# Performance work log

Hardware: AMD Instinct MI355X
Metric: run time of the kernel (lower is better)

Reference implementation:

```python
import jax, jax.numpy as jnp
import numpy as np

B, CIN, COUT, H, W = 2, 64, 64, 192, 192
G = 2          # offset groups (region + semantic offset branches concatenated)
KK = 9         # 3x3 kernel taps
CG = CIN // G  # channels per offset group


def conv2d(x, w, b):
    # NCHW, OIHW, stride 1, padding 1 (same as nn.Conv2d(k=3, s=1, p=1))
    y = jax.lax.conv_general_dilated(x, w, (1, 1), ((1, 1), (1, 1)),
                                     dimension_numbers=('NCHW', 'OIHW', 'NCHW'))
    return y + b[None, :, None, None]


def bilinear_gather(x, py, px):
    # x: (B,G,C,H,W); py,px: (B,G,K,H,W) absolute sample coords (float)
    b, g, c, h, w = x.shape
    k = py.shape[2]
    y0 = jnp.floor(py)
    x0 = jnp.floor(px)
    ly = (py - y0)[:, :, None]   # (B,G,1,K,H,W)
    lx = (px - x0)[:, :, None]
    xf = x.reshape(b, g, c, h * w)

    def corner(yi, xi):
        valid = (yi >= 0) & (yi < h) & (xi >= 0) & (xi < w)
        idx = (jnp.clip(yi, 0, h - 1).astype(jnp.int32) * w
               + jnp.clip(xi, 0, w - 1).astype(jnp.int32))          # (B,G,K,H,W)
        idxf = idx.reshape(b, g, k * h * w)
        gat = jax.vmap(jax.vmap(lambda xc, ic: jnp.take(xc, ic, axis=1)))(xf, idxf)
        gat = gat.reshape(b, g, c, k, h, w)
        return gat * valid[:, :, None].astype(x.dtype)

    v00 = corner(y0, x0)
    v01 = corner(y0, x0 + 1)
    v10 = corner(y0 + 1, x0)
    v11 = corner(y0 + 1, x0 + 1)
    return (v00 * (1 - ly) * (1 - lx) + v01 * (1 - ly) * lx
            + v10 * ly * (1 - lx) + v11 * ly * lx)


def setup_inputs() -> dict:
    key = jax.random.key(0)
    ks = jax.random.split(key, 12)
    stdv = 1.0 / np.sqrt(CIN * 9)
    inp = {
        'input': jax.random.normal(ks[0], (B, CIN, H, W), jnp.float32),
        'mask_in': jax.random.uniform(ks[1], (B, 1, H, W), jnp.float32),
        'weight': jax.random.uniform(ks[2], (COUT, CIN, 3, 3), jnp.float32, -stdv, stdv),
        'bias': jnp.zeros((COUT,), jnp.float32),
        'sem_w': jax.random.normal(ks[3], (2 * KK, CIN, 3, 3), jnp.float32) * 0.01,
        'sem_b': jnp.zeros((2 * KK,), jnp.float32),
        'reg_w': jax.random.normal(ks[4], (2 * KK, 1, 3, 3), jnp.float32) * 0.01,
        'reg_b': jnp.zeros((2 * KK,), jnp.float32),
        'm1_w': jax.random.normal(ks[5], (KK, 1, 3, 3), jnp.float32) * 0.1,
        'm1_b': jnp.zeros((KK,), jnp.float32),
        'm2_w': jax.random.normal(ks[6], (KK, CIN, 3, 3), jnp.float32) * 0.1,
        'm2_b': jnp.zeros((KK,), jnp.float32),
    }
    return inp


def reference(input, mask_in, weight, bias, sem_w, sem_b, reg_w, reg_b,
              m1_w, m1_b, m2_w, m2_b):
    f32 = input.dtype
    # --- learned offsets: region (group 0) then semantic (group 1) ---
    region_offset = conv2d(mask_in, reg_w, reg_b)    # (B, 2*9, H, W)
    semantic_offset = conv2d(input, sem_w, sem_b)    # (B, 2*9, H, W)
    offset = jnp.concatenate([region_offset, semantic_offset], axis=1)
    off = offset.reshape(B, G, KK, 2, H, W)          # [..., 0]=dy, [..., 1]=dx
    ky = (jnp.arange(KK) // 3 - 1).astype(f32)[None, None, :, None, None]
    kx = (jnp.arange(KK) % 3 - 1).astype(f32)[None, None, :, None, None]
    gy = jnp.arange(H, dtype=f32)[None, None, None, :, None]
    gx = jnp.arange(W, dtype=f32)[None, None, None, None, :]
    py = off[:, :, :, 0] + gy + ky                   # (B,G,K,H,W)
    px = off[:, :, :, 1] + gx + kx

    # --- update mask: deform conv of repeated mask with all-ones weight (no grad) ---
    # mask repeated over CIN channels -> identical within each offset group, so
    # sample one channel per group and scale: out = 2 (out chans) * CG * sum_{g,k}
    mgrp = jnp.broadcast_to(mask_in[:, None], (B, G, 1, H, W))
    sm = bilinear_gather(mgrp, py, px)               # (B,G,1,K,H,W)
    update_mask = jnp.clip(2.0 * CG * sm.sum(axis=(1, 2, 3)), 0.0, 1.0)[:, None]
    update_mask = jax.lax.stop_gradient(update_mask)  # (B,1,H,W)

    # --- modulation masks ---
    dm1 = jax.nn.sigmoid(conv2d(mask_in, m1_w, m1_b))  # (B,9,H,W) -> group 0
    dm2 = jax.nn.sigmoid(conv2d(input, m2_w, m2_b))    # (B,9,H,W) -> group 1
    dmask = jnp.concatenate([dm1, dm2], axis=1).reshape(B, G, KK, H, W)[:, :, None]

    # --- main modulated deformable conv ---
    xg = input.reshape(B, G, CG, H, W)
    sampled = bilinear_gather(xg, py, px) * dmask    # (B,G,CG,K,H,W)
    wr = weight.reshape(COUT, G, CG, KK)
    raw = jnp.einsum('bgckhw,ogck->bohw', sampled, wr) + bias[None, :, None, None]

    output = raw * update_mask
    return output, update_mask
```

## Files before the change

kernel.cpp:

```cpp
#include <hip/hip_runtime.h>
#include <hip/hip_bf16.h>
#include <math.h>

#define B_  2
#define CIN 64
#define COUT 64
#define H_  192
#define W_  192
#define G_  2
#define KK_ 9
#define CG_ 32
#define HW_ (H_*W_)
#define PIX 32
#define XT_ (W_/PIX)
#define PR_ 7
#define PC_ 38
#define PST 72
#define NB_NHWC (B_ * (HW_ / 64))
#define NB_WT   ((18*4*64*8 + 18*2*64*8) / 256)

typedef __attribute__((ext_vector_type(8))) short bf16x8;
typedef __attribute__((ext_vector_type(4))) float f32x4;

static __device__ __forceinline__ short f2bf(float f) {
    unsigned u = __builtin_bit_cast(unsigned, f);
    u = (u + 0x7fffu + ((u >> 16) & 1u)) >> 16;
    return (short)u;
}
static __device__ __forceinline__ float bf2f(short s) {
    unsigned u = ((unsigned)(unsigned short)s) << 16;
    return __builtin_bit_cast(float, u);
}
static __device__ __forceinline__ short2 pk2bf(float lo, float hi) {
    float2 f; f.x = lo; f.y = hi;
    __hip_bfloat162 hh = __float22bfloat162_rn(f);
    short2 r;
    __builtin_memcpy(&r, &hh, sizeof(r));
    return r;
}

__global__ __launch_bounds__(256)
void prep_kernel(const float* __restrict__ in,
                 const float* __restrict__ weight,
                 const float* __restrict__ sem_w,
                 const float* __restrict__ m2_w,
                 short* __restrict__ inpT,
                 short* __restrict__ wbm,
                 short* __restrict__ wbs) {
    __shared__ float t[64][65];
    const int tid = threadIdx.x;
    const int bid = blockIdx.x;
    if (bid < NB_NHWC) {
        const int b = bid / (HW_ / 64);
        const int pix0 = (bid % (HW_ / 64)) * 64;
        const float* src = in + (size_t)b * CIN * HW_ + pix0;
        const int c0 = (tid >> 6) * 16;
        const int p  = tid & 63;
        #pragma unroll
        for (int i = 0; i < 16; ++i)
            t[c0 + i][p] = src[(size_t)(c0 + i) * HW_ + p];
        __syncthreads();
        short* dst = inpT + ((size_t)b * HW_ + pix0) * 64;
        #pragma unroll
        for (int i = 0; i < 2; ++i) {
            int item = i * 256 + tid;
            int pp = item >> 3, oct = item & 7;
            bf16x8 v;
            #pragma unroll
            for (int j = 0; j < 8; j += 2) {
                short2 ss = pk2bf(t[oct * 8 + j][pp], t[oct * 8 + j + 1][pp]);
                v[j] = ss.x; v[j + 1] = ss.y;
            }
            *(bf16x8*)&dst[pp * 64 + oct * 8] = v;
        }
        return;
    }
    int i = (bid - NB_NHWC) * 256 + tid;
    if (i < 18 * 4 * 64 * 8) {
        int j = i & 7, lane = (i >> 3) & 63, nt = (i >> 9) & 3, gk = i >> 11;
        int n = lane & 15, q = lane >> 4;
        int o = nt * 16 + n;
        int g = gk / 9, k = gk - g * 9;
        int cin = g * CG_ + q * 8 + j;
        wbm[i] = f2bf(weight[(o * CIN + cin) * 9 + k]);
        return;
    }
    int ii = i - 18 * 4 * 64 * 8;
    if (ii >= 18 * 2 * 64 * 8) return;
    int j = ii & 7, lane = (ii >> 3) & 63, nt = (ii >> 9) & 1, s = ii >> 10;
    int t_ = s >> 1, h = s & 1;
    int n = lane & 15, q = lane >> 4;
    int o = nt * 16 + n;
    int c = h * 32 + q * 8 + j;
    float v = 0.f;
    if (o < 18)      v = sem_w[(o * CIN + c) * 9 + t_];
    else if (o < 27) v = m2_w[((o - 18) * CIN + c) * 9 + t_];
    wbs[ii] = f2bf(v);
}

#define MSTEP(GK) { \
    uint4 mt0 = meta[(GK) * 32 + n]; \
    uint4 mt1 = meta[(GK) * 32 + 16 + n]; \
    const short* pb = patch + team * 32 + q * 8; \
    bf16x8 d00 = *(const bf16x8*)&pb[(mt0.z & 0xffffu) * PST]; \
    bf16x8 d01 = *(const bf16x8*)&pb[(mt0.z >> 16) * PST]; \
    bf16x8 d10 = *(const bf16x8*)&pb[(mt0.w & 0xffffu) * PST]; \
    bf16x8 d11 = *(const bf16x8*)&pb[(mt0.w >> 16) * PST]; \
    bf16x8 e00 = *(const bf16x8*)&pb[(mt1.z & 0xffffu) * PST]; \
    bf16x8 e01 = *(const bf16x8*)&pb[(mt1.z >> 16) * PST]; \
    bf16x8 e10 = *(const bf16x8*)&pb[(mt1.w & 0xffffu) * PST]; \
    bf16x8 e11 = *(const bf16x8*)&pb[(mt1.w >> 16) * PST]; \
    float v00 = bf2f((short)(mt0.x & 0xffffu)); \
    float v01 = bf2f((short)(mt0.x >> 16)); \
    float v10 = bf2f((short)(mt0.y & 0xffffu)); \
    float v11 = bf2f((short)(mt0.y >> 16)); \
    float u00 = bf2f((short)(mt1.x & 0xffffu)); \
    float u01 = bf2f((short)(mt1.x >> 16)); \
    float u10 = bf2f((short)(mt1.y & 0xffffu)); \
    float u11 = bf2f((short)(mt1.y >> 16)); \
    bf16x8 a0, a1; \
    _Pragma("unroll") \
    for (int j = 0; j < 8; j += 2) { \
        float s0 = v00 * bf2f(d00[j])   + v01 * bf2f(d01[j]) \
                 + v10 * bf2f(d10[j])   + v11 * bf2f(d11[j]); \
        float s1 = v00 * bf2f(d00[j+1]) + v01 * bf2f(d01[j+1]) \
                 + v10 * bf2f(d10[j+1]) + v11 * bf2f(d11[j+1]); \
        short2 ss = pk2bf(s0, s1); \
        a0[j] = ss.x; a0[j + 1] = ss.y; \
        float t0 = u00 * bf2f(e00[j])   + u01 * bf2f(e01[j]) \
                 + u10 * bf2f(e10[j])   + u11 * bf2f(e11[j]); \
        float t1 = u00 * bf2f(e00[j+1]) + u01 * bf2f(e01[j+1]) \
                 + u10 * bf2f(e10[j+1]) + u11 * bf2f(e11[j+1]); \
        short2 tt = pk2bf(t0, t1); \
        a1[j] = tt.x; a1[j + 1] = tt.y; \
    } \
    bf16x8 wb0 = ((const bf16x8*)wbm)[((GK) * 4 + 0) * 64 + lane]; \
    bf16x8 wb1 = ((const bf16x8*)wbm)[((GK) * 4 + 1) * 64 + lane]; \
    bf16x8 wb2 = ((const bf16x8*)wbm)[((GK) * 4 + 2) * 64 + lane]; \
    bf16x8 wb3 = ((const bf16x8*)wbm)[((GK) * 4 + 3) * 64 + lane]; \
    ma00 = __builtin_amdgcn_mfma_f32_16x16x32_bf16(a0, wb0, ma00, 0, 0, 0); \
    ma01 = __builtin_amdgcn_mfma_f32_16x16x32_bf16(a0, wb1, ma01, 0, 0, 0); \
    ma02 = __builtin_amdgcn_mfma_f32_16x16x32_bf16(a0, wb2, ma02, 0, 0, 0); \
    ma03 = __builtin_amdgcn_mfma_f32_16x16x32_bf16(a0, wb3, ma03, 0, 0, 0); \
    ma10 = __builtin_amdgcn_mfma_f32_16x16x32_bf16(a1, wb0, ma10, 0, 0, 0); \
    ma11 = __builtin_amdgcn_mfma_f32_16x16x32_bf16(a1, wb1, ma11, 0, 0, 0); \
    ma12 = __builtin_amdgcn_mfma_f32_16x16x32_bf16(a1, wb2, ma12, 0, 0, 0); \
    ma13 = __builtin_amdgcn_mfma_f32_16x16x32_bf16(a1, wb3, ma13, 0, 0, 0); \
}

#define DUMP(OP) { \
    _Pragma("unroll") \
    for (int r = 0; r < 4; ++r) { \
        dout[(q * 4 + r) * 68 +  0 + n] OP ma00[r]; \
        dout[(q * 4 + r) * 68 + 16 + n] OP ma01[r]; \
        dout[(q * 4 + r) * 68 + 32 + n] OP ma02[r]; \
        dout[(q * 4 + r) * 68 + 48 + n] OP ma03[r]; \
        dout[(16 + q * 4 + r) * 68 +  0 + n] OP ma10[r]; \
        dout[(16 + q * 4 + r) * 68 + 16 + n] OP ma11[r]; \
        dout[(16 + q * 4 + r) * 68 + 32 + n] OP ma12[r]; \
        dout[(16 + q * 4 + r) * 68 + 48 + n] OP ma13[r]; \
    } \
}

__global__ __launch_bounds__(256)
void fused_kernel(const short* __restrict__ inpT,
                  const float* __restrict__ mask_in,
                  const short* __restrict__ wbs,
                  const short* __restrict__ wbm,
                  const float* __restrict__ sem_b,
                  const float* __restrict__ reg_w, const float* __restrict__ reg_b,
                  const float* __restrict__ m1_w, const float* __restrict__ m1_b,
                  const float* __restrict__ m2_b,
                  const float* __restrict__ bias,
                  float* __restrict__ out, float* __restrict__ um_out) {
    __shared__ __align__(16) short patch[PR_ * PC_ * PST];
    __shared__ __align__(16) char sh[9216];
    __shared__ uint4 meta[18 * 32];
    __shared__ float ums[4 * 32];
    __shared__ float umv[32];
    float* red  = (float*)sh;
    float* dout = (float*)sh;

    const int tid  = threadIdx.x;
    const int lane = tid & 63;
    const int w    = __builtin_amdgcn_readfirstlane(tid >> 6);
    const int team = w >> 1;
    const int kh   = w & 1;
    const int n = lane & 15, q = lane >> 4;

    const int bid  = blockIdx.x;
    const int band = bid & 7;
    const int jb   = bid >> 3;
    const int xt   = jb % XT_;
    const int rr   = band * 48 + jb / XT_;
    const int y    = rr % H_;
    const int b    = rr / H_;
    const int x0   = xt * PIX;

    for (int i = tid; i < PR_ * PC_ * 8; i += 256) {
        int chunk = i & 7;
        int cc = (i >> 3) % PC_;
        int rp = (i >> 3) / PC_;
        int yy = y - 3 + rp;
        int xx = x0 - 3 + cc;
        bf16x8 v = {0, 0, 0, 0, 0, 0, 0, 0};
        if (yy >= 0 && yy < H_ && xx >= 0 && xx < W_)
            v = *(const bf16x8*)&inpT[((size_t)(b * HW_ + yy * W_ + xx)) * 64 + chunk * 8];
        *(bf16x8*)&patch[(rp * PC_ + cc) * PST + chunk * 8] = v;
    }
    __syncthreads();

    f32x4 acc0 = {0.f, 0.f, 0.f, 0.f}, acc1 = {0.f, 0.f, 0.f, 0.f};
    for (int ss = 0; ss < 9; ++ss) {
        int s = team * 9 + ss;
        int tt = s >> 1, hh = s & 1;
        int dy = tt / 3 - 1, dx = tt % 3 - 1;
        int r = dy + 3;
        int c = kh * 16 + n + dx + 3;
        bf16x8 a = *(const bf16x8*)&patch[(r * PC_ + c) * PST + hh * 32 + q * 8];
        bf16x8 b0 = ((const bf16x8*)wbs)[(s * 2 + 0) * 64 + lane];
        bf16x8 b1 = ((const bf16x8*)wbs)[(s * 2 + 1) * 64 + lane];
        acc0 = __builtin_amdgcn_mfma_f32_16x16x32_bf16(a, b0, acc0, 0, 0, 0);
        acc1 = __builtin_amdgcn_mfma_f32_16x16x32_bf16(a, b1, acc1, 0, 0, 0);
    }
    #pragma unroll
    for (int r = 0; r < 4; ++r) {
        red[team * 1152 + (kh * 16 + q * 4 + r) * 36 + n]      = acc0[r];
        red[team * 1152 + (kh * 16 + q * 4 + r) * 36 + 16 + n] = acc1[r];
    }
    __syncthreads();

    if (w < 2) {
        const int g    = w;
        const int half = lane >> 5;
        const int pxl  = lane & 31;
        const int xl   = x0 + pxl;
        const int pixl = y * W_ + xl;
        const bool vxm = xl > 0, vxp = (xl + 1) < W_;
        const bool vym = y > 0,  vyp = (y + 1) < H_;
        const int k0 = half ? 5 : 0;
        const int k1 = half ? 9 : 5;
        float off_[18], mm[9];
        if (g == 0) {
            const float* mbp = mask_in + (size_t)b * HW_ + pixl;
            float mv[9];
            mv[0] = (vym && vxm) ? mbp[-W_ - 1] : 0.f;
            mv[1] = vym ? mbp[-W_] : 0.f;
            mv[2] = (vym && vxp) ? mbp[-W_ + 1] : 0.f;
            mv[3] = vxm ? mbp[-1] : 0.f;
            mv[4] = mbp[0];
            mv[5] = vxp ? mbp[1] : 0.f;
            mv[6] = (vyp && vxm) ? mbp[W_ - 1] : 0.f;
            mv[7] = vyp ? mbp[W_] : 0.f;
            mv[8] = (vyp && vxp) ? mbp[W_ + 1] : 0.f;
            #pragma unroll
            for (int o = 0; o < 18; ++o) off_[o] = reg_b[o];
            #pragma unroll
            for (int o = 0; o < 9; ++o) mm[o] = m1_b[o];
            #pragma unroll
            for (int t = 0; t < 9; ++t) {
                float vt = mv[t];
                #pragma unroll
                for (int o = 0; o < 18; ++o) off_[o] += vt * reg_w[o * 9 + t];
                #pragma unroll
                for (int o = 0; o < 9; ++o) mm[o] += vt * m1_w[o * 9 + t];
            }
        } else {
            #pragma unroll
            for (int o = 0; o < 18; ++o)
                off_[o] = red[pxl * 36 + o] + red[1152 + pxl * 36 + o] + sem_b[o];
            #pragma unroll
            for (int o = 0; o < 9; ++o)
                mm[o] = red[pxl * 36 + 18 + o] + red[1152 + pxl * 36 + 18 + o] + m2_b[o];
        }

        const float* mb = mask_in + (size_t)b * HW_;
        float s_um = 0.f;
        #pragma unroll
        for (int k = 0; k < 9; ++k) {
            if (k < k0 || k >= k1) continue;
            float Y = off_[2 * k]     + (float)y  + (float)(k / 3 - 1);
            float X = off_[2 * k + 1] + (float)xl + (float)(k % 3 - 1);
            int gk = g * 9 + k;
            float dm = 1.f / (1.f + expf(-mm[k]));
            float y0f = floorf(Y), x0f = floorf(X);
            int yi0 = (int)y0f, xi0 = (int)x0f;
            float ly = Y - y0f, lx = X - x0f;
            int yi1 = yi0 + 1, xi1 = xi0 + 1;
            bool vy0 = (yi0 >= 0 && yi0 < H_), vy1 = (yi1 >= 0 && yi1 < H_);
            bool vx0 = (xi0 >= 0 && xi0 < W_), vx1 = (xi1 >= 0 && xi1 < W_);
            float w00f = (vy0 && vx0) ? (1.f - ly) * (1.f - lx) : 0.f;
            float w01f = (vy0 && vx1) ? (1.f - ly) * lx : 0.f;
            float w10f = (vy1 && vx0) ? ly * (1.f - lx) : 0.f;
            float w11f = (vy1 && vx1) ? ly * lx : 0.f;
            int yc0 = min(max(yi0, 0), H_ - 1), yc1 = min(max(yi1, 0), H_ - 1);
            int xc0 = min(max(xi0, 0), W_ - 1), xc1 = min(max(xi1, 0), W_ - 1);
            s_um += w00f * mb[yc0 * W_ + xc0] + w01f * mb[yc0 * W_ + xc1]
                  + w10f * mb[yc1 * W_ + xc0] + w11f * mb[yc1 * W_ + xc1];
            int r0 = min(max(yc0 - (y - 3), 0), PR_ - 1);
            int r1 = min(max(yc1 - (y - 3), 0), PR_ - 1);
            int c0 = min(max(xc0 - (x0 - 3), 0), PC_ - 1);
            int c1 = min(max(xc1 - (x0 - 3), 0), PC_ - 1);
            short2 p01 = pk2bf(w00f * dm, w01f * dm);
            short2 p23 = pk2bf(w10f * dm, w11f * dm);
            uint4 mt;
            mt.x = (unsigned)(unsigned short)p01.x | ((unsigned)(unsigned short)p01.y << 16);
            mt.y = (unsigned)(unsigned short)p23.x | ((unsigned)(unsigned short)p23.y << 16);
            mt.z = (unsigned)(r0 * PC_ + c0) | ((unsigned)(r0 * PC_ + c1) << 16);
            mt.w = (unsigned)(r1 * PC_ + c0) | ((unsigned)(r1 * PC_ + c1) << 16);
            meta[gk * 32 + pxl] = mt;
        }
        ums[(g * 2 + half) * 32 + pxl] = s_um;
    }
    __syncthreads();
    if (tid < 32) {
        float s = ums[tid] + ums[32 + tid] + ums[64 + tid] + ums[96 + tid];
        float u = fminf(fmaxf(64.f * s, 0.f), 1.f);
        um_out[(size_t)b * HW_ + y * W_ + x0 + tid] = u;
        umv[tid] = u;
    }
    __syncthreads();

    f32x4 ma00 = {0.f,0.f,0.f,0.f}, ma01 = {0.f,0.f,0.f,0.f};
    f32x4 ma02 = {0.f,0.f,0.f,0.f}, ma03 = {0.f,0.f,0.f,0.f};
    f32x4 ma10 = {0.f,0.f,0.f,0.f}, ma11 = {0.f,0.f,0.f,0.f};
    f32x4 ma12 = {0.f,0.f,0.f,0.f}, ma13 = {0.f,0.f,0.f,0.f};
    {
        const int t9 = team * 9;
        if (kh == 0) {
            MSTEP(t9 + 0) MSTEP(t9 + 1) MSTEP(t9 + 2) MSTEP(t9 + 3) MSTEP(t9 + 4)
        } else {
            MSTEP(t9 + 5) MSTEP(t9 + 6) MSTEP(t9 + 7) MSTEP(t9 + 8)
        }
    }

    if (w == 3) DUMP(=)
    __syncthreads();
    if (w == 2) DUMP(+=)
    __syncthreads();
    if (w == 1) DUMP(+=)
    __syncthreads();
    if (w == 0) DUMP(+=)
    __syncthreads();

    {
        const int pxs = tid & 31;
        const int o0  = (tid >> 5) * 8;
        float u = umv[pxs];
        float* ob = out + ((size_t)b * COUT + o0) * HW_ + y * W_ + x0 + pxs;
        const float* bs = bias + o0;
        const float* dp = &dout[pxs * 68 + o0];
        #pragma unroll
        for (int o = 0; o < 8; ++o)
            ob[(size_t)o * HW_] = (dp[o] + bs[o]) * u;
    }
}

extern "C" void kernel_launch(void* const* d_in, const int* in_sizes, int n_in,
                              void* d_out, int out_size, void* d_ws, size_t ws_size,
                              hipStream_t stream) {
    const float* input   = (const float*)d_in[0];
    const float* mask_in = (const float*)d_in[1];
    const float* weight  = (const float*)d_in[2];
    const float* bias    = (const float*)d_in[3];
    const float* sem_w   = (const float*)d_in[4];
    const float* sem_b   = (const float*)d_in[5];
    const float* reg_w   = (const float*)d_in[6];
    const float* reg_b   = (const float*)d_in[7];
    const float* m1_w    = (const float*)d_in[8];
    const float* m1_b    = (const float*)d_in[9];
    const float* m2_w    = (const float*)d_in[10];
    const float* m2_b    = (const float*)d_in[11];

    float* out = (float*)d_out;
    float* um  = out + (size_t)B_ * COUT * HW_;

    short* inpT = (short*)d_ws;
    short* wbm  = inpT + (size_t)B_ * HW_ * 64;
    short* wbs  = wbm + 18 * 4 * 64 * 8;

    prep_kernel<<<NB_NHWC + NB_WT, 256, 0, stream>>>(
        input, weight, sem_w, m2_w, inpT, wbm, wbs);
    fused_kernel<<<B_ * H_ * XT_, 256, 0, stream>>>(
        inpT, mask_in, wbs, wbm, sem_b, reg_w, reg_b, m1_w, m1_b, m2_b,
        bias, out, um);
}
```

Before: 151.5 us.

## Switch to fp16 with packed half2 bilinear math and restructure meta/reduction

Converts input and weight staging from bf16 to fp16 so the bilinear interpolation runs as packed half2 FMAs and the MFMAs use the f16 variant. Shrinks per-sample metadata to packed half weights plus a single 16-bit patch index, deriving the other three corners from fixed offsets. Spreads offset/meta computation across all four waves instead of two, and replaces the serialized four-step accumulation dump with per-wave slices reused in the patch buffer and summed in the epilogue. It also switches to fast exp and reduces mask sums with a shuffle. Risks include fp16 range and precision loss, and clamping the corner index to PR-2/PC-2 may differ at borders.

New measurement: 139.5 us. -7.9%, faster.

```diff
diff --git a/kernel.cpp b/kernel.cpp
--- a/kernel.cpp
+++ b/kernel.cpp
@@ -1,5 +1,5 @@
 #include <hip/hip_runtime.h>
-#include <hip/hip_bf16.h>
+#include <hip/hip_fp16.h>
 #include <math.h>
 
 #define B_  2
@@ -16,27 +16,35 @@
 #define PR_ 7
 #define PC_ 38
 #define PST 72
+#define DSTR 69
 #define NB_NHWC (B_ * (HW_ / 64))
 #define NB_WT   ((18*4*64*8 + 18*2*64*8) / 256)
 
 typedef __attribute__((ext_vector_type(8))) short bf16x8;
+typedef __attribute__((ext_vector_type(8))) _Float16 f16x8;
+typedef __attribute__((ext_vector_type(4))) unsigned int u32x4;
 typedef __attribute__((ext_vector_type(4))) float f32x4;
 
-static __device__ __forceinline__ short f2bf(float f) {
-    unsigned u = __builtin_bit_cast(unsigned, f);
-    u = (u + 0x7fffu + ((u >> 16) & 1u)) >> 16;
-    return (short)u;
-}
-static __device__ __forceinline__ float bf2f(short s) {
-    unsigned u = ((unsigned)(unsigned short)s) << 16;
-    return __builtin_bit_cast(float, u);
-}
-static __device__ __forceinline__ short2 pk2bf(float lo, float hi) {
-    float2 f; f.x = lo; f.y = hi;
-    __hip_bfloat162 hh = __float22bfloat162_rn(f);
-    short2 r;
-    __builtin_memcpy(&r, &hh, sizeof(r));
-    return r;
+static __device__ __forceinline__ short f2h(float f) {
+    _Float16 h = (_Float16)f;
+    return __builtin_bit_cast(short, h);
+}
+static __device__ __forceinline__ unsigned pk2hu(float lo, float hi) {
+    auto h = __builtin_amdgcn_cvt_pkrtz(lo, hi);
+    return __builtin_bit_cast(unsigned, h);
+}
+static __device__ __forceinline__ short2 pk2h(float lo, float hi) {
+    auto h = __builtin_amdgcn_cvt_pkrtz(lo, hi);
+    return __builtin_bit_cast(short2, h);
+}
+static __device__ __forceinline__ __half2 bcl(unsigned u) {
+    return __builtin_bit_cast(__half2, (unsigned)((u & 0xffffu) | (u << 16)));
+}
+static __device__ __forceinline__ __half2 bch(unsigned u) {
+    return __builtin_bit_cast(__half2, (unsigned)((u >> 16) | (u & 0xffff0000u)));
+}
+static __device__ __forceinline__ __half2 H2(unsigned u) {
+    return __builtin_bit_cast(__half2, u);
 }
 
 __global__ __launch_bounds__(256)
@@ -68,7 +76,7 @@
             bf16x8 v;
             #pragma unroll
             for (int j = 0; j < 8; j += 2) {
-                short2 ss = pk2bf(t[oct * 8 + j][pp], t[oct * 8 + j + 1][pp]);
+                short2 ss = pk2h(t[oct * 8 + j][pp], t[oct * 8 + j + 1][pp]);
                 v[j] = ss.x; v[j + 1] = ss.y;
             }
             *(bf16x8*)&dst[pp * 64 + oct * 8] = v;
@@ -82,7 +90,7 @@
         int o = nt * 16 + n;
         int g = gk / 9, k = gk - g * 9;
         int cin = g * CG_ + q * 8 + j;
-        wbm[i] = f2bf(weight[(o * CIN + cin) * 9 + k]);
+        wbm[i] = f2h(weight[(o * CIN + cin) * 9 + k]);
         return;
     }
     int ii = i - 18 * 4 * 64 * 8;
@@ -95,70 +103,63 @@
     float v = 0.f;
     if (o < 18)      v = sem_w[(o * CIN + c) * 9 + t_];
     else if (o < 27) v = m2_w[((o - 18) * CIN + c) * 9 + t_];
-    wbs[ii] = f2bf(v);
+    wbs[ii] = f2h(v);
 }
 
 #define MSTEP(GK) { \
-    uint4 mt0 = meta[(GK) * 32 + n]; \
-    uint4 mt1 = meta[(GK) * 32 + 16 + n]; \
+    const uint2 mw0 = meta_w[(GK) * 32 + n]; \
+    const uint2 mw1 = meta_w[(GK) * 32 + 16 + n]; \
+    const int i0 = (int)meta_i[(GK) * 32 + n] * PST; \
+    const int i1 = (int)meta_i[(GK) * 32 + 16 + n] * PST; \
     const short* pb = patch + team * 32 + q * 8; \
-    bf16x8 d00 = *(const bf16x8*)&pb[(mt0.z & 0xffffu) * PST]; \
-    bf16x8 d01 = *(const bf16x8*)&pb[(mt0.z >> 16) * PST]; \
-    bf16x8 d10 = *(const bf16x8*)&pb[(mt0.w & 0xffffu) * PST]; \
-    bf16x8 d11 = *(const bf16x8*)&pb[(mt0.w >> 16) * PST]; \
-    bf16x8 e00 = *(const bf16x8*)&pb[(mt1.z & 0xffffu) * PST]; \
-    bf16x8 e01 = *(const bf16x8*)&pb[(mt1.z >> 16) * PST]; \
-    bf16x8 e10 = *(const bf16x8*)&pb[(mt1.w & 0xffffu) * PST]; \
-    bf16x8 e11 = *(const bf16x8*)&pb[(mt1.w >> 16) * PST]; \
-    float v00 = bf2f((short)(mt0.x & 0xffffu)); \
-    float v01 = bf2f((short)(mt0.x >> 16)); \
-    float v10 = bf2f((short)(mt0.y & 0xffffu)); \
-    float v11 = bf2f((short)(mt0.y >> 16)); \
-    float u00 = bf2f((short)(mt1.x & 0xffffu)); \
-    float u01 = bf2f((short)(mt1.x >> 16)); \
-    float u10 = bf2f((short)(mt1.y & 0xffffu)); \
-    float u11 = bf2f((short)(mt1.y >> 16)); \
-    bf16x8 a0, a1; \
+    u32x4 d00 = *(const u32x4*)&pb[i0]; \
+    u32x4 d01 = *(const u32x4*)&pb[i0 + PST]; \
+    u32x4 d10 = *(const u32x4*)&pb[i0 + PC_ * PST]; \
+    u32x4 d11 = *(const u32x4*)&pb[i0 + (PC_ + 1) * PST]; \
+    u32x4 e00 = *(const u32x4*)&pb[i1]; \
+    u32x4 e01 = *(const u32x4*)&pb[i1 + PST]; \
+    u32x4 e10 = *(const u32x4*)&pb[i1 + PC_ * PST]; \
+    u32x4 e11 = *(const u32x4*)&pb[i1 + (PC_ + 1) * PST]; \
+    __half2 v00 = bcl(mw0.x), v01 = bch(mw0.x), v10 = bcl(mw0.y), v11 = bch(mw0.y); \
+    __half2 u00 = bcl(mw1.x), u01 = bch(mw1.x), u10 = bcl(mw1.y), u11 = bch(mw1.y); \
+    u32x4 ra, rb; \
     _Pragma("unroll") \
-    for (int j = 0; j < 8; j += 2) { \
-        float s0 = v00 * bf2f(d00[j])   + v01 * bf2f(d01[j]) \
-                 + v10 * bf2f(d10[j])   + v11 * bf2f(d11[j]); \
-        float s1 = v00 * bf2f(d00[j+1]) + v01 * bf2f(d01[j+1]) \
-                 + v10 * bf2f(d10[j+1]) + v11 * bf2f(d11[j+1]); \
-        short2 ss = pk2bf(s0, s1); \
-        a0[j] = ss.x; a0[j + 1] = ss.y; \
-        float t0 = u00 * bf2f(e00[j])   + u01 * bf2f(e01[j]) \
-                 + u10 * bf2f(e10[j])   + u11 * bf2f(e11[j]); \
-        float t1 = u00 * bf2f(e00[j+1]) + u01 * bf2f(e01[j+1]) \
-                 + u10 * bf2f(e10[j+1]) + u11 * bf2f(e11[j+1]); \
-        short2 tt = pk2bf(t0, t1); \
-        a1[j] = tt.x; a1[j + 1] = tt.y; \
+    for (int jj = 0; jj < 4; ++jj) { \
+        __half2 s = __hfma2(H2(d00[jj]), v00, __hfma2(H2(d01[jj]), v01, \
+                    __hfma2(H2(d10[jj]), v10, __hmul2(H2(d11[jj]), v11)))); \
+        ra[jj] = __builtin_bit_cast(unsigned, s); \
+        __half2 t = __hfma2(H2(e00[jj]), u00, __hfma2(H2(e01[jj]), u01, \
+                    __hfma2(H2(e10[jj]), u10, __hmul2(H2(e11[jj]), u11)))); \
+        rb[jj] = __builtin_bit_cast(unsigned, t); \
     } \
-    bf16x8 wb0 = ((const bf16x8*)wbm)[((GK) * 4 + 0) * 64 + lane]; \
-    bf16x8 wb1 = ((const bf16x8*)wbm)[((GK) * 4 + 1) * 64 + lane]; \
-    bf16x8 wb2 = ((const bf16x8*)wbm)[((GK) * 4 + 2) * 64 + lane]; \
-    bf16x8 wb3 = ((const bf16x8*)wbm)[((GK) * 4 + 3) * 64 + lane]; \
-    ma00 = __builtin_amdgcn_mfma_f32_16x16x32_bf16(a0, wb0, ma00, 0, 0, 0); \
-    ma01 = __builtin_amdgcn_mfma_f32_16x16x32_bf16(a0, wb1, ma01, 0, 0, 0); \
-    ma02 = __builtin_amdgcn_mfma_f32_16x16x32_bf16(a0, wb2, ma02, 0, 0, 0); \
-    ma03 = __builtin_amdgcn_mfma_f32_16x16x32_bf16(a0, wb3, ma03, 0, 0, 0); \
-    ma10 = __builtin_amdgcn_mfma_f32_16x16x32_bf16(a1, wb0, ma10, 0, 0, 0); \
-    ma11 = __builtin_amdgcn_mfma_f32_16x16x32_bf16(a1, wb1, ma11, 0, 0, 0); \
-    ma12 = __builtin_amdgcn_mfma_f32_16x16x32_bf16(a1, wb2, ma12, 0, 0, 0); \
-    ma13 = __builtin_amdgcn_mfma_f32_16x16x32_bf16(a1, wb3, ma13, 0, 0, 0); \
-}
-
-#define DUMP(OP) { \
+    f16x8 a0 = __builtin_bit_cast(f16x8, ra); \
+    f16x8 a1 = __builtin_bit_cast(f16x8, rb); \
+    f16x8 wb0 = ((const f16x8*)wbm)[((GK) * 4 + 0) * 64 + lane]; \
+    f16x8 wb1 = ((const f16x8*)wbm)[((GK) * 4 + 1) * 64 + lane]; \
+    f16x8 wb2 = ((const f16x8*)wbm)[((GK) * 4 + 2) * 64 + lane]; \
+    f16x8 wb3 = ((const f16x8*)wbm)[((GK) * 4 + 3) * 64 + lane]; \
+    ma00 = __builtin_amdgcn_mfma_f32_16x16x32_f16(a0, wb0, ma00, 0, 0, 0); \
+    ma01 = __builtin_amdgcn_mfma_f32_16x16x32_f16(a0, wb1, ma01, 0, 0, 0); \
+    ma02 = __builtin_amdgcn_mfma_f32_16x16x32_f16(a0, wb2, ma02, 0, 0, 0); \
+    ma03 = __builtin_amdgcn_mfma_f32_16x16x32_f16(a0, wb3, ma03, 0, 0, 0); \
+    ma10 = __builtin_amdgcn_mfma_f32_16x16x32_f16(a1, wb0, ma10, 0, 0, 0); \
+    ma11 = __builtin_amdgcn_mfma_f32_16x16x32_f16(a1, wb1, ma11, 0, 0, 0); \
+    ma12 = __builtin_amdgcn_mfma_f32_16x16x32_f16(a1, wb2, ma12, 0, 0, 0); \
+    ma13 = __builtin_amdgcn_mfma_f32_16x16x32_f16(a1, wb3, ma13, 0, 0, 0); \
+}
+
+#define DUMP() { \
+    float* dw = dout + w * (32 * DSTR); \
     _Pragma("unroll") \
     for (int r = 0; r < 4; ++r) { \
-        dout[(q * 4 + r) * 68 +  0 + n] OP ma00[r]; \
-        dout[(q * 4 + r) * 68 + 16 + n] OP ma01[r]; \
-        dout[(q * 4 + r) * 68 + 32 + n] OP ma02[r]; \
-        dout[(q * 4 + r) * 68 + 48 + n] OP ma03[r]; \
-        dout[(16 + q * 4 + r) * 68 +  0 + n] OP ma10[r]; \
-        dout[(16 + q * 4 + r) * 68 + 16 + n] OP ma11[r]; \
-        dout[(16 + q * 4 + r) * 68 + 32 + n] OP ma12[r]; \
-        dout[(16 + q * 4 + r) * 68 + 48 + n] OP ma13[r]; \
+        dw[(q * 4 + r) * DSTR +  0 + n] = ma00[r]; \
+        dw[(q * 4 + r) * DSTR + 16 + n] = ma01[r]; \
+        dw[(q * 4 + r) * DSTR + 32 + n] = ma02[r]; \
+        dw[(q * 4 + r) * DSTR + 48 + n] = ma03[r]; \
+        dw[(16 + q * 4 + r) * DSTR +  0 + n] = ma10[r]; \
+        dw[(16 + q * 4 + r) * DSTR + 16 + n] = ma11[r]; \
+        dw[(16 + q * 4 + r) * DSTR + 32 + n] = ma12[r]; \
+        dw[(16 + q * 4 + r) * DSTR + 48 + n] = ma13[r]; \
     } \
 }
 
@@ -174,12 +175,12 @@
                   const float* __restrict__ bias,
                   float* __restrict__ out, float* __restrict__ um_out) {
     __shared__ __align__(16) short patch[PR_ * PC_ * PST];
-    __shared__ __align__(16) char sh[9216];
-    __shared__ uint4 meta[18 * 32];
+    __shared__ __align__(16) float red[2 * 32 * 36];
+    __shared__ __align__(8) uint2 meta_w[18 * 32];
+    __shared__ unsigned short meta_i[18 * 32];
     __shared__ float ums[4 * 32];
     __shared__ float umv[32];
-    float* red  = (float*)sh;
-    float* dout = (float*)sh;
+    float* dout = (float*)patch;
 
     const int tid  = threadIdx.x;
     const int lane = tid & 63;
@@ -217,11 +218,11 @@
         int dy = tt / 3 - 1, dx = tt % 3 - 1;
         int r = dy + 3;
         int c = kh * 16 + n + dx + 3;
-        bf16x8 a = *(const bf16x8*)&patch[(r * PC_ + c) * PST + hh * 32 + q * 8];
-        bf16x8 b0 = ((const bf16x8*)wbs)[(s * 2 + 0) * 64 + lane];
-        bf16x8 b1 = ((const bf16x8*)wbs)[(s * 2 + 1) * 64 + lane];
-        acc0 = __builtin_amdgcn_mfma_f32_16x16x32_bf16(a, b0, acc0, 0, 0, 0);
-        acc1 = __builtin_amdgcn_mfma_f32_16x16x32_bf16(a, b1, acc1, 0, 0, 0);
+        f16x8 a = *(const f16x8*)&patch[(r * PC_ + c) * PST + hh * 32 + q * 8];
+        f16x8 b0 = ((const f16x8*)wbs)[(s * 2 + 0) * 64 + lane];
+        f16x8 b1 = ((const f16x8*)wbs)[(s * 2 + 1) * 64 + lane];
+        acc0 = __builtin_amdgcn_mfma_f32_16x16x32_f16(a, b0, acc0, 0, 0, 0);
+        acc1 = __builtin_amdgcn_mfma_f32_16x16x32_f16(a, b1, acc1, 0, 0, 0);
     }
     #pragma unroll
     for (int r = 0; r < 4; ++r) {
@@ -230,16 +231,17 @@
     }
     __syncthreads();
 
-    if (w < 2) {
-        const int g    = w;
+    {
+        const int g    = team;
         const int half = lane >> 5;
         const int pxl  = lane & 31;
         const int xl   = x0 + pxl;
         const int pixl = y * W_ + xl;
         const bool vxm = xl > 0, vxp = (xl + 1) < W_;
         const bool vym = y > 0,  vyp = (y + 1) < H_;
-        const int k0 = half ? 5 : 0;
-        const int k1 = half ? 9 : 5;
+        const int qk = (kh << 1) | half;
+        const int k0 = (qk == 0) ? 0 : (qk == 1) ? 3 : (qk == 2) ? 5 : 7;
+        const int k1 = (qk == 0) ? 3 : (qk == 1) ? 5 : (qk == 2) ? 7 : 9;
         float off_[18], mm[9];
         if (g == 0) {
             const float* mbp = mask_in + (size_t)b * HW_ + pixl;
@@ -282,7 +284,7 @@
             float Y = off_[2 * k]     + (float)y  + (float)(k / 3 - 1);
             float X = off_[2 * k + 1] + (float)xl + (float)(k % 3 - 1);
             int gk = g * 9 + k;
-            float dm = 1.f / (1.f + expf(-mm[k]));
+            float dm = 1.f / (1.f + __expf(-mm[k]));
             float y0f = floorf(Y), x0f = floorf(X);
             int yi0 = (int)y0f, xi0 = (int)x0f;
             float ly = Y - y0f, lx = X - x0f;
@@ -297,27 +299,14 @@
             int xc0 = min(max(xi0, 0), W_ - 1), xc1 = min(max(xi1, 0), W_ - 1);
             s_um += w00f * mb[yc0 * W_ + xc0] + w01f * mb[yc0 * W_ + xc1]
                   + w10f * mb[yc1 * W_ + xc0] + w11f * mb[yc1 * W_ + xc1];
-            int r0 = min(max(yc0 - (y - 3), 0), PR_ - 1);
-            int r1 = min(max(yc1 - (y - 3), 0), PR_ - 1);
-            int c0 = min(max(xc0 - (x0 - 3), 0), PC_ - 1);
-            int c1 = min(max(xc1 - (x0 - 3), 0), PC_ - 1);
-            short2 p01 = pk2bf(w00f * dm, w01f * dm);
-            short2 p23 = pk2bf(w10f * dm, w11f * dm);
-            uint4 mt;
-            mt.x = (unsigned)(unsigned short)p01.x | ((unsigned)(unsigned short)p01.y << 16);
-            mt.y = (unsigned)(unsigned short)p23.x | ((unsigned)(unsigned short)p23.y << 16);
-            mt.z = (unsigned)(r0 * PC_ + c0) | ((unsigned)(r0 * PC_ + c1) << 16);
-            mt.w = (unsigned)(r1 * PC_ + c0) | ((unsigned)(r1 * PC_ + c1) << 16);
-            meta[gk * 32 + pxl] = mt;
+            int r0 = min(max(yi0 - (y - 3), 0), PR_ - 2);
+            int c0 = min(max(xi0 - (x0 - 3), 0), PC_ - 2);
+            meta_w[gk * 32 + pxl] = make_uint2(pk2hu(w00f * dm, w01f * dm),
+                                               pk2hu(w10f * dm, w11f * dm));
+            meta_i[gk * 32 + pxl] = (unsigned short)(r0 * PC_ + c0);
         }
-        ums[(g * 2 + half) * 32 + pxl] = s_um;
-    }
-    __syncthreads();
-    if (tid < 32) {
-        float s = ums[tid] + ums[32 + tid] + ums[64 + tid] + ums[96 + tid];
-        float u = fminf(fmaxf(64.f * s, 0.f), 1.f);
-        um_out[(size_t)b * HW_ + y * W_ + x0 + tid] = u;
-        umv[tid] = u;
+        s_um += __shfl_xor(s_um, 32);
+        if (half == 0) ums[w * 32 + pxl] = s_um;
     }
     __syncthreads();
 
@@ -333,14 +322,15 @@
             MSTEP(t9 + 5) MSTEP(t9 + 6) MSTEP(t9 + 7) MSTEP(t9 + 8)
         }
     }
-
-    if (w == 3) DUMP(=)
-    __syncthreads();
-    if (w == 2) DUMP(+=)
-    __syncthreads();
-    if (w == 1) DUMP(+=)
-    __syncthreads();
-    if (w == 0) DUMP(+=)
+    __syncthreads();
+
+    DUMP();
+    if (tid < 32) {
+        float s = ums[tid] + ums[32 + tid] + ums[64 + tid] + ums[96 + tid];
+        float u = fminf(fmaxf(64.f * s, 0.f), 1.f);
+        um_out[(size_t)b * HW_ + y * W_ + x0 + tid] = u;
+        umv[tid] = u;
+    }
     __syncthreads();
 
     {
@@ -349,10 +339,11 @@
         float u = umv[pxs];
         float* ob = out + ((size_t)b * COUT + o0) * HW_ + y * W_ + x0 + pxs;
         const float* bs = bias + o0;
-        const float* dp = &dout[pxs * 68 + o0];
+        const float* dp = dout + pxs * DSTR + o0;
         #pragma unroll
         for (int o = 0; o < 8; ++o)
-            ob[(size_t)o * HW_] = (dp[o] + bs[o]) * u;
+            ob[(size_t)o * HW_] = (dp[o] + dp[32 * DSTR + o] + dp[2 * 32 * DSTR + o]
+                                   + dp[3 * 32 * DSTR + o] + bs[o]) * u;
     }
 }
 
```
